# Optimization experiments

Hardware: AMD Instinct MI355X
Metric: run time of the kernel (lower is better)

## Reference

```python
import jax, jax.numpy as jnp
import numpy as np

NUM_GRAPHS = 256


def _mean_aggregate(h, src, dst, num_nodes):
    # DGL copy_src + mean reduce: dst node gets mean of src-node features over in-edges.
    summed = jax.ops.segment_sum(h[src], dst, num_segments=num_nodes)  # [N, F]
    deg = jax.ops.segment_sum(jnp.ones((src.shape[0],), h.dtype), dst, num_segments=num_nodes)
    return summed / jnp.maximum(deg, 1.0)[:, None]


def setup_inputs() -> dict:
    key = jax.random.key(0)
    ks = jax.random.split(key, 10)
    N, E, D_IN, H1, H2, OUT = 50000, 800000, 128, 256, 128, 1
    s = lambda fan: 1.0 / np.sqrt(fan)
    return {
        "h": jax.random.normal(ks[0], (N, D_IN), jnp.float32),
        "src": jax.random.randint(ks[1], (E,), 0, N),
        "dst": jax.random.randint(ks[2], (E,), 0, N),
        "graph_ids": jnp.sort(jax.random.randint(ks[3], (N,), 0, NUM_GRAPHS)),
        "W1": jax.random.normal(ks[4], (D_IN, H1), jnp.float32) * s(D_IN),
        "b1": jnp.zeros((H1,), jnp.float32),
        "W2": jax.random.normal(ks[5], (H1, H1), jnp.float32) * s(H1),
        "b2": jnp.zeros((H1,), jnp.float32),
        "Wr1": jax.random.normal(ks[6], (H1, H2), jnp.float32) * s(H1),
        "br1": jnp.zeros((H2,), jnp.float32),
        "Wr2": jax.random.normal(ks[7], (H2, OUT), jnp.float32) * s(H2),
        "br2": jnp.zeros((OUT,), jnp.float32),
    }


def reference(h, src, dst, graph_ids, W1, b1, W2, b2, Wr1, br1, Wr2, br2):
    N = h.shape[0]
    # GCN layer 1: mean-aggregate then linear+ReLU
    h = _mean_aggregate(h, src, dst, N)
    h = jax.nn.relu(h @ W1 + b1)
    # GCN layer 2
    h = _mean_aggregate(h, src, dst, N)
    h = jax.nn.relu(h @ W2 + b2)
    # dgl.mean_nodes readout: per-graph mean of node features
    gsum = jax.ops.segment_sum(h, graph_ids, num_segments=NUM_GRAPHS)  # [G, H1]
    gcnt = jax.ops.segment_sum(jnp.ones((N,), h.dtype), graph_ids, num_segments=NUM_GRAPHS)
    hg = gsum / jnp.maximum(gcnt, 1.0)[:, None]
    hidden = hg @ Wr1 + br1
    return hidden @ Wr2 + br2  # [G, 1]
```

## Files before the change

### kernel.cpp

```cpp
#include <hip/hip_runtime.h>


#define NUM_GRAPHS 256
#define MAXDEG 64

#define CNT_B0 0
#define CNT_NB 1024
#define CST_B0 (CNT_B0 + CNT_NB)
#define CST_NB 512
#define GST_B0 (CST_B0 + CST_NB)
#define GST_NB 64
#define WT1_B0 (GST_B0 + GST_NB)
#define WT1_NB 16
#define WT2_B0 (WT1_B0 + WT1_NB)
#define WT2_NB 32
#define MISC_NB (WT2_B0 + WT2_NB)

typedef __attribute__((ext_vector_type(8))) short bf16x8;
typedef __attribute__((ext_vector_type(4))) float f32x4;

__device__ inline unsigned short f2bf(float f) {
    unsigned u = __float_as_uint(f);
    return (unsigned short)((u + 0x7fff + ((u >> 16) & 1)) >> 16);
}
__device__ inline float bflo(unsigned u) { return __uint_as_float(u << 16); }
__device__ inline float bfhi(unsigned u) { return __uint_as_float(u & 0xffff0000u); }


__launch_bounds__(256)
__global__ void misc_kernel(const int* __restrict__ dst, const int* __restrict__ src,
                            const int* __restrict__ gids,
                            const float* __restrict__ h,
                            const float* __restrict__ W1, const float* __restrict__ W2,
                            int* __restrict__ cnt, unsigned short* __restrict__ eidx,
                            int* __restrict__ gstart,
                            unsigned short* __restrict__ hb,
                            unsigned short* __restrict__ Wt1, unsigned short* __restrict__ Wt2,
                            int N, int E) {
    int b = blockIdx.x, tid = threadIdx.x;
    if (b < CST_B0) {
        int lid = (b - CNT_B0) * 256 + tid;
        for (int e = lid; e < E; e += CNT_NB * 256) {
            int d = __builtin_nontemporal_load(&dst[e]);
            int s = __builtin_nontemporal_load(&src[e]);
            int r = atomicAdd(&cnt[d], 1);
            if (r < MAXDEG)
                eidx[(size_t)d * MAXDEG + r] = (unsigned short)s;
        }
    } else if (b < GST_B0) {
        int lid = (b - CST_B0) * 256 + tid;
        int total4 = N * 32;
        for (int i = lid; i < total4; i += CST_NB * 256) {
            float4 v = *(const float4*)(h + (size_t)i * 4);
            ushort4 o;
            o.x = f2bf(v.x); o.y = f2bf(v.y); o.z = f2bf(v.z); o.w = f2bf(v.w);
            *(ushort4*)(hb + (size_t)i * 4) = o;
        }
    } else if (b < WT1_B0) {
        int lid = (b - GST_B0) * 256 + tid;
        for (int n = lid; n < N; n += GST_NB * 256) {
            int g = gids[n];
            int gp = (n == 0) ? -1 : gids[n - 1];
            for (int x = gp + 1; x <= g; ++x) gstart[x] = n;
            if (n == N - 1)
                for (int x = g + 1; x <= NUM_GRAPHS; ++x) gstart[x] = N;
        }
    } else if (b < WT2_B0) {
        int lid = (b - WT1_B0) * 256 + tid;
        for (int i = lid; i < 256 * 128; i += WT1_NB * 256)
            Wt1[i] = f2bf(W1[(size_t)(i & 127) * 256 + (i >> 7)]);
    } else {
        int lid = (b - WT2_B0) * 256 + tid;
        for (int i = lid; i < 256 * 256; i += WT2_NB * 256)
            Wt2[i] = f2bf(W2[(size_t)(i & 255) * 256 + (i >> 8)]);
    }
}


template <int D>
__global__ void agg_mean_bf16_kernel(const unsigned short* __restrict__ feat,
                                     const int* __restrict__ cnt,
                                     const unsigned short* __restrict__ eidx,
                                     unsigned short* __restrict__ out, int N) {
    constexpr int VPL = D / 64;
    int wave = blockIdx.x * (blockDim.x >> 6) + (threadIdx.x >> 6);
    int lane = threadIdx.x & 63;
    if (wave >= N) return;
    int deg = cnt[wave];
    int stored = deg > MAXDEG ? MAXDEG : deg;
    const unsigned short* row = eidx + (size_t)wave * MAXDEG;
    int myIdx = (lane < stored) ? (int)row[lane] : 0;

    float acc[VPL];
    #pragma unroll
    for (int i = 0; i < VPL; ++i) acc[i] = 0.0f;

    int j = 0;
    for (; j + 8 <= stored; j += 8) {
        if constexpr (VPL == 2) {
            unsigned v[8];
            #pragma unroll
            for (int u = 0; u < 8; ++u) {
                int s = __shfl(myIdx, j + u, 64);
                v[u] = *(const unsigned*)(feat + (size_t)s * D + lane * 2);
            }
            #pragma unroll
            for (int u = 0; u < 8; ++u) { acc[0] += bflo(v[u]); acc[1] += bfhi(v[u]); }
        } else {
            uint2 v[8];
            #pragma unroll
            for (int u = 0; u < 8; ++u) {
                int s = __shfl(myIdx, j + u, 64);
                v[u] = *(const uint2*)(feat + (size_t)s * D + lane * 4);
            }
            #pragma unroll
            for (int u = 0; u < 8; ++u) {
                acc[0] += bflo(v[u].x); acc[1] += bfhi(v[u].x);
                acc[2] += bflo(v[u].y); acc[3] += bfhi(v[u].y);
            }
        }
    }
    for (; j < stored; ++j) {
        int s = __shfl(myIdx, j, 64);
        if constexpr (VPL == 2) {
            unsigned v = *(const unsigned*)(feat + (size_t)s * D + lane * 2);
            acc[0] += bflo(v); acc[1] += bfhi(v);
        } else {
            uint2 v = *(const uint2*)(feat + (size_t)s * D + lane * 4);
            acc[0] += bflo(v.x); acc[1] += bfhi(v.x);
            acc[2] += bflo(v.y); acc[3] += bfhi(v.y);
        }
    }

    float invd = 1.0f / (float)(deg > 0 ? deg : 1);
    if constexpr (VPL == 2) {
        unsigned o = (unsigned)f2bf(acc[0] * invd) | ((unsigned)f2bf(acc[1] * invd) << 16);
        __builtin_nontemporal_store(o, (unsigned*)(out + (size_t)wave * D + lane * 2));
    } else {
        unsigned lo = (unsigned)f2bf(acc[0] * invd) | ((unsigned)f2bf(acc[1] * invd) << 16);
        unsigned hi = (unsigned)f2bf(acc[2] * invd) | ((unsigned)f2bf(acc[3] * invd) << 16);
        unsigned long long o = (unsigned long long)lo | ((unsigned long long)hi << 32);
        __builtin_nontemporal_store(o, (unsigned long long*)(out + (size_t)wave * D + lane * 4));
    }
}


template <int K, int MODE>
__launch_bounds__(256)
__global__ void gemm_mfma_kernel(const unsigned short* __restrict__ A,
                                 const unsigned short* __restrict__ Wt,
                                 const float* __restrict__ bias,
                                 unsigned short* __restrict__ Cb,
                                 const int* __restrict__ gids,
                                 float* __restrict__ gsum,
                                 int N) {
    constexpr int LDS = 40;
    __shared__ unsigned short As[64 * LDS];
    __shared__ unsigned short Bs[256 * LDS];

    int tid = threadIdx.x;
    int wave = tid >> 6;
    int lane = tid & 63;
    int m = lane & 15;
    int q = lane >> 4;
    int rowBase = blockIdx.x * 64;

    f32x4 acc[4][4] = {};

    for (int kc = 0; kc < K; kc += 32) {
        {
            int r = tid >> 2;
            int seg = tid & 3;
            int gr = rowBase + r;
            uint4 v = make_uint4(0, 0, 0, 0);
            if (gr < N) v = *(const uint4*)(A + (size_t)gr * K + kc + seg * 8);
            *(uint4*)&As[r * LDS + seg * 8] = v;
        }
        #pragma unroll
        for (int it = 0; it < 4; ++it) {
            int n = (tid >> 2) + it * 64;
            int seg = tid & 3;
            uint4 v = *(const uint4*)(Wt + (size_t)n * K + kc + seg * 8);
            *(uint4*)&Bs[n * LDS + seg * 8] = v;
        }
        __syncthreads();

        bf16x8 af[4], bfr[4];
        #pragma unroll
        for (int r = 0; r < 4; ++r)
            af[r] = *(const bf16x8*)&As[(r * 16 + m) * LDS + q * 8];
        #pragma unroll
        for (int c = 0; c < 4; ++c)
            bfr[c] = *(const bf16x8*)&Bs[(wave * 64 + c * 16 + m) * LDS + q * 8];
        #pragma unroll
        for (int r = 0; r < 4; ++r)
            #pragma unroll
            for (int c = 0; c < 4; ++c)
                acc[r][c] = __builtin_amdgcn_mfma_f32_16x16x32_bf16(af[r], bfr[c], acc[r][c], 0, 0, 0);
        __syncthreads();
    }

    if constexpr (MODE == 0) {
        #pragma unroll
        for (int c = 0; c < 4; ++c) {
            int col = wave * 64 + c * 16 + m;
            float bv = bias[col];
            #pragma unroll
            for (int r = 0; r < 4; ++r) {
                #pragma unroll
                for (int reg = 0; reg < 4; ++reg) {
                    int grow = rowBase + r * 16 + q * 4 + reg;
                    if (grow < N)
                        Cb[(size_t)grow * 256 + col] = f2bf(fmaxf(acc[r][c][reg] + bv, 0.0f));
                }
            }
        }
    } else {
        int* sgid = (int*)As;
        if (tid < 64) {
            int gr = rowBase + tid;
            sgid[tid] = (gr < N) ? gids[gr] : 0x7fffffff;
        }
        __syncthreads();
        int lastValid = N - 1 - rowBase;
        if (lastValid > 63) lastValid = 63;
        int gmin = sgid[0];
        int gmax = sgid[lastValid];
        #pragma unroll
        for (int c = 0; c < 4; ++c) {
            int col = wave * 64 + c * 16 + m;
            float bv = bias[col];
            for (int g = gmin; g <= gmax; ++g) {
                float p = 0.0f;
                #pragma unroll
                for (int r = 0; r < 4; ++r) {
                    #pragma unroll
                    for (int reg = 0; reg < 4; ++reg) {
                        int lr = r * 16 + q * 4 + reg;
                        if (sgid[lr] == g)
                            p += fmaxf(acc[r][c][reg] + bv, 0.0f);
                    }
                }
                p += __shfl_xor(p, 16, 64);
                p += __shfl_xor(p, 32, 64);
                if (q == 0 && p != 0.0f)
                    atomicAdd(&gsum[g * 256 + col], p);
            }
        }
    }
}


__global__ void final_kernel(const float* __restrict__ gsum, const int* __restrict__ gstart,
                             const float* __restrict__ Wr1, const float* __restrict__ br1,
                             const float* __restrict__ Wr2, const float* __restrict__ br2,
                             float* __restrict__ out) {
    __shared__ float part[512];
    __shared__ float ws2[2];
    int g = blockIdx.x;
    int t = threadIdx.x;
    int j = t & 127;
    int kq = t >> 7;
    int c = gstart[g + 1] - gstart[g];
    float invc = 1.0f / (float)(c > 0 ? c : 1);
    const float* gs = gsum + g * 256;
    float acc = 0.0f;
    #pragma unroll 8
    for (int k = kq * 64; k < kq * 64 + 64; ++k)
        acc += gs[k] * Wr1[k * 128 + j];
    part[t] = acc;
    __syncthreads();
    if (t < 128) {
        float s = part[j] + part[128 + j] + part[256 + j] + part[384 + j];
        float p = (s * invc + br1[j]) * Wr2[j];
        #pragma unroll
        for (int d = 32; d > 0; d >>= 1) p += __shfl_down(p, d, 64);
        if ((t & 63) == 0) ws2[t >> 6] = p;
    }
    __syncthreads();
    if (t == 0) out[g] = ws2[0] + ws2[1] + br2[0];
}


extern "C" void kernel_launch(void* const* d_in, const int* in_sizes, int n_in,
                              void* d_out, int out_size, void* d_ws, size_t ws_size,
                              hipStream_t stream) {
    const float* h    = (const float*)d_in[0];
    const int*   src  = (const int*)d_in[1];
    const int*   dst  = (const int*)d_in[2];
    const int*   gids = (const int*)d_in[3];
    const float* W1   = (const float*)d_in[4];
    const float* b1   = (const float*)d_in[5];
    const float* W2   = (const float*)d_in[6];
    const float* b2   = (const float*)d_in[7];
    const float* Wr1  = (const float*)d_in[8];
    const float* br1  = (const float*)d_in[9];
    const float* Wr2  = (const float*)d_in[10];
    const float* br2  = (const float*)d_in[11];

    int N = in_sizes[0] / 128;
    int E = in_sizes[1];

    char* w = (char*)d_ws;
    unsigned short* hb     = (unsigned short*)w;  w += (size_t)N * 128 * sizeof(unsigned short);
    unsigned short* h1b    = (unsigned short*)w;  w += (size_t)N * 256 * sizeof(unsigned short);
    unsigned short* aggOut = (unsigned short*)w;  w += (size_t)N * 256 * sizeof(unsigned short);
    int* cnt    = (int*)w;              w += (size_t)N * sizeof(int);
    float* gsum = (float*)w;            w += (size_t)NUM_GRAPHS * 256 * sizeof(float);
    unsigned short* eidx = (unsigned short*)w;  w += (size_t)N * MAXDEG * sizeof(unsigned short);
    unsigned short* Wt1 = (unsigned short*)w;   w += 256 * 128 * sizeof(unsigned short);
    unsigned short* Wt2 = (unsigned short*)w;   w += 256 * 256 * sizeof(unsigned short);
    int* gstart = (int*)w;              w += (size_t)(NUM_GRAPHS + 1) * sizeof(int);

    hipMemsetAsync(cnt, 0,
                   (size_t)N * sizeof(int) + (size_t)NUM_GRAPHS * 256 * sizeof(float),
                   stream);
    misc_kernel<<<MISC_NB, 256, 0, stream>>>(dst, src, gids, h, W1, W2, cnt, eidx,
                                             gstart, hb, Wt1, Wt2, N, E);

    agg_mean_bf16_kernel<128><<<(N + 3) / 4, 256, 0, stream>>>(hb, cnt, eidx, aggOut, N);
    gemm_mfma_kernel<128, 0><<<(N + 63) / 64, 256, 0, stream>>>(aggOut, Wt1, b1, h1b, nullptr, nullptr, N);

    agg_mean_bf16_kernel<256><<<(N + 3) / 4, 256, 0, stream>>>(h1b, cnt, eidx, aggOut, N);
    gemm_mfma_kernel<256, 1><<<(N + 63) / 64, 256, 0, stream>>>(aggOut, Wt2, b2, nullptr, gids, gsum, N);

    final_kernel<<<NUM_GRAPHS, 512, 0, stream>>>(gsum, gstart, Wr1, br1, Wr2, br2, (float*)d_out);
}
```

Measured before the change: 283.7 us.

## Build adjacency lists via two-pass bucket partition instead of global atomics

Replaces per-edge global atomicAdd on per-node counters with a two-level scheme. Edges are first partitioned into buckets of 512 destination nodes, using shared-memory histograms and one global cursor atomic per bucket per block, and packed src/dst-local words are written to a scratch buffer that reuses aggOut. A new build kernel then fills each bucket's per-node edge lists and counts with shared-memory atomics. This is meant to cut contended, scattered global atomics, at the cost of an extra kernel launch, an extra pass over dst, and a fixed bucket capacity (GCAP) that silently drops edges if exceeded.

```diff
diff --git a/kernel.cpp b/kernel.cpp
--- a/kernel.cpp
+++ b/kernel.cpp
@@ -3,10 +3,12 @@
 
 #define NUM_GRAPHS 256
 #define MAXDEG 64
-
-#define CNT_B0 0
-#define CNT_NB 1024
-#define CST_B0 (CNT_B0 + CNT_NB)
+#define GSHIFT 9
+#define GCAP 9216
+
+#define PART_B0 0
+#define PART_NB 256
+#define CST_B0 (PART_B0 + PART_NB)
 #define CST_NB 512
 #define GST_B0 (CST_B0 + CST_NB)
 #define GST_NB 64
@@ -32,20 +34,41 @@
                             const int* __restrict__ gids,
                             const float* __restrict__ h,
                             const float* __restrict__ W1, const float* __restrict__ W2,
-                            int* __restrict__ cnt, unsigned short* __restrict__ eidx,
+                            int* __restrict__ cursor, unsigned* __restrict__ partE,
                             int* __restrict__ gstart,
                             unsigned short* __restrict__ hb,
                             unsigned short* __restrict__ Wt1, unsigned short* __restrict__ Wt2,
                             int N, int E) {
     int b = blockIdx.x, tid = threadIdx.x;
     if (b < CST_B0) {
-        int lid = (b - CNT_B0) * 256 + tid;
-        for (int e = lid; e < E; e += CNT_NB * 256) {
+        __shared__ unsigned lcnt[128];
+        __shared__ unsigned gb[128];
+        int ngrp = (N + 511) >> GSHIFT;
+        int b0 = b - PART_B0;
+        int chunk = (E + PART_NB - 1) / PART_NB;
+        int ebeg = b0 * chunk;
+        int eend = ebeg + chunk; if (eend > E) eend = E;
+        for (int i = tid; i < 128; i += 256) lcnt[i] = 0;
+        __syncthreads();
+        for (int e = ebeg + tid; e < eend; e += 256) {
+            int d = __builtin_nontemporal_load(&dst[e]);
+            atomicAdd(&lcnt[d >> GSHIFT], 1u);
+        }
+        __syncthreads();
+        for (int g = tid; g < ngrp; g += 256) {
+            unsigned c = lcnt[g];
+            gb[g] = c ? (unsigned)atomicAdd(&cursor[g], (int)c) : 0u;
+            lcnt[g] = 0;
+        }
+        __syncthreads();
+        for (int e = ebeg + tid; e < eend; e += 256) {
             int d = __builtin_nontemporal_load(&dst[e]);
             int s = __builtin_nontemporal_load(&src[e]);
-            int r = atomicAdd(&cnt[d], 1);
-            if (r < MAXDEG)
-                eidx[(size_t)d * MAXDEG + r] = (unsigned short)s;
+            int g = d >> GSHIFT;
+            unsigned r = atomicAdd(&lcnt[g], 1u) + gb[g];
+            if (r < GCAP)
+                __builtin_nontemporal_store(((unsigned)s << GSHIFT) | (unsigned)(d & 511),
+                                            &partE[(size_t)g * GCAP + r]);
         }
     } else if (b < GST_B0) {
         int lid = (b - CST_B0) * 256 + tid;
@@ -73,6 +96,33 @@
         int lid = (b - WT2_B0) * 256 + tid;
         for (int i = lid; i < 256 * 256; i += WT2_NB * 256)
             Wt2[i] = f2bf(W2[(size_t)(i & 255) * 256 + (i >> 8)]);
+    }
+}
+
+
+__launch_bounds__(256)
+__global__ void build_kernel(const unsigned* __restrict__ partE,
+                             const int* __restrict__ cursor,
+                             int* __restrict__ cnt, unsigned short* __restrict__ eidx,
+                             int N) {
+    __shared__ unsigned hist[512];
+    int g = blockIdx.x, tid = threadIdx.x;
+    for (int i = tid; i < 512; i += 256) hist[i] = 0;
+    __syncthreads();
+    int ec = cursor[g]; if (ec > GCAP) ec = GCAP;
+    const unsigned* pe = partE + (size_t)g * GCAP;
+    for (int i = tid; i < ec; i += 256) {
+        unsigned p = pe[i];
+        int dl = (int)(p & 511);
+        int s = (int)(p >> GSHIFT);
+        unsigned r = atomicAdd(&hist[dl], 1u);
+        if (r < MAXDEG)
+            eidx[((size_t)((g << GSHIFT) + dl)) * MAXDEG + r] = (unsigned short)s;
+    }
+    __syncthreads();
+    for (int i = tid; i < 512; i += 256) {
+        int node = (g << GSHIFT) + i;
+        if (node < N) cnt[node] = (int)hist[i];
     }
 }
 
@@ -300,6 +350,7 @@
 
     int N = in_sizes[0] / 128;
     int E = in_sizes[1];
+    int ngrp = (N + 511) >> GSHIFT;
 
     char* w = (char*)d_ws;
     unsigned short* hb     = (unsigned short*)w;  w += (size_t)N * 128 * sizeof(unsigned short);
@@ -307,16 +358,19 @@
     unsigned short* aggOut = (unsigned short*)w;  w += (size_t)N * 256 * sizeof(unsigned short);
     int* cnt    = (int*)w;              w += (size_t)N * sizeof(int);
     float* gsum = (float*)w;            w += (size_t)NUM_GRAPHS * 256 * sizeof(float);
+    int* cursor = (int*)w;              w += 128 * sizeof(int);
     unsigned short* eidx = (unsigned short*)w;  w += (size_t)N * MAXDEG * sizeof(unsigned short);
     unsigned short* Wt1 = (unsigned short*)w;   w += 256 * 128 * sizeof(unsigned short);
     unsigned short* Wt2 = (unsigned short*)w;   w += 256 * 256 * sizeof(unsigned short);
     int* gstart = (int*)w;              w += (size_t)(NUM_GRAPHS + 1) * sizeof(int);
-
-    hipMemsetAsync(cnt, 0,
-                   (size_t)N * sizeof(int) + (size_t)NUM_GRAPHS * 256 * sizeof(float),
+    unsigned* partE = (unsigned*)aggOut;
+
+    hipMemsetAsync(gsum, 0,
+                   (size_t)NUM_GRAPHS * 256 * sizeof(float) + 128 * sizeof(int),
                    stream);
-    misc_kernel<<<MISC_NB, 256, 0, stream>>>(dst, src, gids, h, W1, W2, cnt, eidx,
+    misc_kernel<<<MISC_NB, 256, 0, stream>>>(dst, src, gids, h, W1, W2, cursor, partE,
                                              gstart, hb, Wt1, Wt2, N, E);
+    build_kernel<<<ngrp, 256, 0, stream>>>(partE, cursor, cnt, eidx, N);
 
     agg_mean_bf16_kernel<128><<<(N + 3) / 4, 256, 0, stream>>>(hb, cnt, eidx, aggOut, N);
     gemm_mfma_kernel<128, 0><<<(N + 63) / 64, 256, 0, stream>>>(aggOut, Wt1, b1, h1b, nullptr, nullptr, N);
```

New measurement: 286.7 us. Within noise of the previous version (+1.1%).
